# Optimization experiments

Measured on AMD Instinct MI355X. Metric: run time of the kernel, lower is better.

Reference implementation:

```python
import jax, jax.numpy as jnp
import numpy as np

DIM = 1024
HEADS = 16
HEAD_DIM = 64
WINDOW = 64


def setup_inputs() -> dict:
    key = jax.random.key(0)
    ks = jax.random.split(key, 9)
    s = lambda fan_in: 1.0 / np.sqrt(fan_in)
    x = jax.random.normal(ks[0], (2, 2048, DIM), dtype=jnp.float32)
    # KANEXLayer: phi = Linear(dim, hidden=dim) -> SiLU -> Linear(dim, dim); g = Linear(dim, 3*H*D)
    W1 = jax.random.uniform(ks[1], (DIM, DIM), jnp.float32, -s(DIM), s(DIM))
    b1 = jax.random.uniform(ks[2], (DIM,), jnp.float32, -s(DIM), s(DIM))
    W2 = jax.random.uniform(ks[3], (DIM, DIM), jnp.float32, -s(DIM), s(DIM))
    b2 = jax.random.uniform(ks[4], (DIM,), jnp.float32, -s(DIM), s(DIM))
    Wg = jax.random.uniform(ks[5], (3 * HEADS * HEAD_DIM, DIM), jnp.float32, -s(DIM), s(DIM))
    bg = jax.random.uniform(ks[6], (3 * HEADS * HEAD_DIM,), jnp.float32, -s(DIM), s(DIM))
    Wo = jax.random.uniform(ks[7], (DIM, HEADS * HEAD_DIM), jnp.float32, -s(HEADS * HEAD_DIM), s(HEADS * HEAD_DIM))
    bo = jax.random.uniform(ks[8], (DIM,), jnp.float32, -s(HEADS * HEAD_DIM), s(HEADS * HEAD_DIM))
    return {"x": x, "W1": W1, "b1": b1, "W2": W2, "b2": b2,
            "Wg": Wg, "bg": bg, "Wo": Wo, "bo": bo}


def reference(x, W1, b1, W2, b2, Wg, bg, Wo, bo):
    b, n, _ = x.shape
    # KANEXLayer: g(phi(x))
    h = jax.nn.silu(x @ W1.T + b1) @ W2.T + b2          # [b, n, dim]
    qkv = h @ Wg.T + bg                                  # [b, n, 3*H*D]
    q, k, v = jnp.split(qkv, 3, axis=-1)
    reshape = lambda t: t.reshape(b, n, HEADS, HEAD_DIM).transpose(0, 2, 1, 3)  # [b, H, n, D]
    q, k, v = reshape(q), reshape(k), reshape(v)
    dots = jnp.einsum('bhid,bhjd->bhij', q, k) * (HEAD_DIM ** -0.5)  # [b, H, n, n]
    # mask positions j >= i + window (triu with diagonal=window_size)
    i = jnp.arange(n)[:, None]
    j = jnp.arange(n)[None, :]
    mask = j >= i + WINDOW                               # [n, n] bool
    dots = jnp.where(mask, -jnp.inf, dots)
    attn = jax.nn.softmax(dots, axis=-1)
    out = jnp.einsum('bhij,bhjd->bhid', attn, v)         # [b, H, n, D]
    out = out.transpose(0, 2, 1, 3).reshape(b, n, HEADS * HEAD_DIM)
    return out @ Wo.T + bo                               # [b, n, dim]
```

## Files before the change

kernel.cpp:

```cpp
#include <hip/hip_runtime.h>

typedef unsigned short u16;
typedef unsigned int   u32;
typedef __bf16 bf16x8 __attribute__((ext_vector_type(8)));
typedef float  f32x4  __attribute__((ext_vector_type(4)));

__device__ __forceinline__ u16 f2bf(float f) {
    return __builtin_bit_cast(u16, (__bf16)f);
}

__device__ __forceinline__ void gload16(const void* g, void* lds) {
    __builtin_amdgcn_global_load_lds(
        (const __attribute__((address_space(1))) u32*)g,
        (__attribute__((address_space(3))) u32*)lds, 16, 0, 0);
}

__device__ __forceinline__ f32x4 mfma16(bf16x8 a, bf16x8 b, f32x4 c) {
    return __builtin_amdgcn_mfma_f32_16x16x32_bf16(a, b, c, 0, 0, 0);
}

__global__ __launch_bounds__(256) void k_cvt5(const float* __restrict__ x,
                                              const float* __restrict__ W1,
                                              const float* __restrict__ W2,
                                              const float* __restrict__ Wg,
                                              const float* __restrict__ Wo,
                                              u16* __restrict__ xb, u16* __restrict__ w1b,
                                              u16* __restrict__ w2b, u16* __restrict__ wgb,
                                              u16* __restrict__ wob) {
    int i = blockIdx.x * 256 + threadIdx.x;
    const float* src; u16* dst; int off;
    if (i < 1048576)      { src = x;  dst = xb;  off = 0; }
    else if (i < 1310720) { src = W1; dst = w1b; off = 1048576; }
    else if (i < 1572864) { src = W2; dst = w2b; off = 1310720; }
    else if (i < 2359296) { src = Wg; dst = wgb; off = 1572864; }
    else                  { src = Wo; dst = wob; off = 2359296; }
    int j = i - off;
    float4 v = ((const float4*)src)[j];
    ushort4 o;
    o.x = f2bf(v.x); o.y = f2bf(v.y); o.z = f2bf(v.z); o.w = f2bf(v.w);
    ((ushort4*)dst)[j] = o;
}

template<bool SILU, bool OUT_BF16>
__global__ __launch_bounds__(512) void k_gemm(const u16* __restrict__ A,
                                              const u16* __restrict__ B,
                                              const float* __restrict__ bias,
                                              void* __restrict__ Cout,
                                              int M, int N, int K, int qcols) {
    __shared__ __align__(16) u16 As[2][128 * 64];
    __shared__ __align__(16) u16 Bs[2][128 * 64];
    const int tid = threadIdx.x;
    const int w = tid >> 6, l = tid & 63;
    const int wm = w >> 2, wn = w & 3;
    const int lr = l & 15, lg = l >> 4;

    const int nwg = gridDim.x * gridDim.y;
    const int hw = blockIdx.x + gridDim.x * blockIdx.y;
    const int wg = (hw & 7) * (nwg >> 3) + (hw >> 3);
    const int m0 = (wg % gridDim.x) * 128, n0 = (wg / gridDim.x) * 128;

    f32x4 acc[4][2];
#pragma unroll
    for (int i = 0; i < 4; ++i)
#pragma unroll
        for (int j = 0; j < 2; ++j) acc[i][j] = (f32x4){0.f, 0.f, 0.f, 0.f};

    const int srow = l >> 3;
    const int ss = (l & 7) ^ (srow & 7);
    auto STAGE = [&](int buf, int kt) {
#pragma unroll
        for (int i = 0; i < 4; ++i) {
            const int g = w * 4 + i;
            if (g < 16)
                gload16(&A[(size_t)(m0 + g * 8 + srow) * K + kt * 64 + ss * 8],
                        &As[buf][g * 512]);
            else
                gload16(&B[(size_t)(n0 + (g - 16) * 8 + srow) * K + kt * 64 + ss * 8],
                        &Bs[buf][(g - 16) * 512]);
        }
    };

    const int nkt = K >> 6;
    STAGE(0, 0);
    __syncthreads();
    for (int kt = 0; kt < nkt; ++kt) {
        const int cur = kt & 1;
        if (kt + 1 < nkt) STAGE(cur ^ 1, kt + 1);
#pragma unroll
        for (int s = 0; s < 2; ++s) {
            bf16x8 af[4], bq[2];
#pragma unroll
            for (int f = 0; f < 4; ++f) {
                const int r = wm * 64 + f * 16 + lr;
                af[f] = *(const bf16x8*)&As[cur][r * 64 + (((s * 4 + lg) ^ (r & 7)) * 8)];
            }
#pragma unroll
            for (int n = 0; n < 2; ++n) {
                const int r = wn * 32 + n * 16 + lr;
                bq[n] = *(const bf16x8*)&Bs[cur][r * 64 + (((s * 4 + lg) ^ (r & 7)) * 8)];
            }
#pragma unroll
            for (int mf = 0; mf < 4; ++mf)
#pragma unroll
                for (int nf = 0; nf < 2; ++nf)
                    acc[mf][nf] = mfma16(af[mf], bq[nf], acc[mf][nf]);
        }
        if (kt + 1 < nkt) __syncthreads();
    }

#pragma unroll
    for (int nf = 0; nf < 2; ++nf) {
        const int col = n0 + wn * 32 + nf * 16 + lr;
        const float bv = bias[col];
        const float cs = (col < qcols) ? 0.18033688011112042f : 1.0f;
#pragma unroll
        for (int mf = 0; mf < 4; ++mf) {
#pragma unroll
            for (int r = 0; r < 4; ++r) {
                const int row = m0 + wm * 64 + mf * 16 + lg * 4 + r;
                float v = acc[mf][nf][r] + bv;
                if (SILU) v = v / (1.0f + __expf(-v));
                v *= cs;
                if (OUT_BF16) ((u16*)Cout)[(size_t)row * N + col] = f2bf(v);
                else          ((float*)Cout)[(size_t)row * N + col] = v;
            }
        }
    }
}

__global__ __launch_bounds__(256) void k_vt(const u16* __restrict__ qkv,
                                            u16* __restrict__ vt) {
    __shared__ u16 tile[64][66];
    const int bh = blockIdx.y;
    const int b = bh >> 4, h = bh & 15;
    const int n0 = blockIdx.x * 64;
    const int tid = threadIdx.x;
#pragma unroll
    for (int it = 0; it < 16; ++it) {
        int idx = it * 256 + tid;
        int r = idx >> 6, c = idx & 63;
        tile[r][c] = qkv[(size_t)(b * 2048 + n0 + r) * 3072 + 2048 + h * 64 + c];
    }
    __syncthreads();
#pragma unroll
    for (int it = 0; it < 16; ++it) {
        int idx = it * 256 + tid;
        int d = idx >> 6, c = idx & 63;
        vt[(size_t)(bh * 64 + d) * 2048 + n0 + c] = tile[c][d];
    }
}

__device__ __forceinline__ void attn_leg(const u16* __restrict__ Ksb,
                                         const u16* __restrict__ Vsb,
                                         u16* __restrict__ Plw,
                                         int lr, int lg, bf16x8 q0, bf16x8 q1,
                                         f32x4 (&o)[4], float& ls,
                                         int thr, bool domask) {
    f32x4 st[4];
#pragma unroll
    for (int f = 0; f < 4; ++f) st[f] = (f32x4){0.f, 0.f, 0.f, 0.f};
    __builtin_amdgcn_s_setprio(1);
#pragma unroll
    for (int s = 0; s < 2; ++s) {
        const bf16x8 qf = s ? q1 : q0;
#pragma unroll
        for (int f = 0; f < 4; ++f) {
            const int row = f * 16 + lr;
            const int sw = ((s * 4 + lg) ^ (row & 7)) * 8;
            bf16x8 kf = *(const bf16x8*)&Ksb[row * 64 + sw];
            st[f] = mfma16(kf, qf, st[f]);
        }
    }
    __builtin_amdgcn_s_setprio(0);
    const int kbase = lg * 4;
#pragma unroll
    for (int f = 0; f < 4; ++f) {
        float pv[4];
#pragma unroll
        for (int r = 0; r < 4; ++r) {
            float sv = st[f][r];
            if (domask) sv = (f * 16 + kbase + r > thr) ? -1e30f : sv;
            pv[r] = exp2f(sv);
            ls += pv[r];
        }
        ushort4 pw;
        pw.x = f2bf(pv[0]); pw.y = f2bf(pv[1]); pw.z = f2bf(pv[2]); pw.w = f2bf(pv[3]);
        *(ushort4*)&Plw[lr * 80 + f * 16 + kbase] = pw;
    }
    __builtin_amdgcn_s_setprio(1);
#pragma unroll
    for (int s = 0; s < 2; ++s) {
        const bf16x8 pf = *(const bf16x8*)&Plw[lr * 80 + s * 32 + lg * 8];
#pragma unroll
        for (int f = 0; f < 4; ++f) {
            const int row = f * 16 + lr;
            const int sw = ((s * 4 + lg) ^ (row & 7)) * 8;
            bf16x8 vf = *(const bf16x8*)&Vsb[row * 64 + sw];
            o[f] = mfma16(pf, vf, o[f]);
        }
    }
    __builtin_amdgcn_s_setprio(0);
}

__global__ __launch_bounds__(512) void k_attn(const u16* __restrict__ qkv,
                                              const u16* __restrict__ vt,
                                              u16* __restrict__ ao) {
    __shared__ __align__(16) u16 Ks[2][64 * 64];
    __shared__ __align__(16) u16 Vs[2][64 * 64];
    __shared__ __align__(16) u16 Pl[8][16 * 80];
    const int hw = blockIdx.x + 16 * blockIdx.y;
    const int logical = (hw & 7) * 64 + (hw >> 3);
    const int p = logical & 15, bh = logical >> 4;
    const int b = bh >> 4, h = bh & 15;
    const int tid = threadIdx.x, w = tid >> 6, l = tid & 63;
    const int lr = l & 15, lg = l >> 4;
    const int i = (w >> 2) ? (31 - p) : p;
    const int nt = min(i + 2, 32);
    const int ntL = min(33 - p, 32);

    const size_t qb = (size_t)(b * 2048 + i * 64 + (w & 3) * 16 + lr) * 3072 + h * 64;
    const bf16x8 q0 = *(const bf16x8*)&qkv[qb + lg * 8];
    const bf16x8 q1 = *(const bf16x8*)&qkv[qb + 32 + lg * 8];

    f32x4 o[4];
#pragma unroll
    for (int f = 0; f < 4; ++f) o[f] = (f32x4){0.f, 0.f, 0.f, 0.f};
    float ls = 0.f;
    const int ql = i * 64 + (w & 3) * 16 + lr;

    const int srow = tid >> 3;
    const int ss = (tid & 7) ^ (srow & 7);
    auto STAGE = [&](int buf, int t) {
        const int j0 = t * 64;
        gload16(&qkv[(size_t)(b * 2048 + j0 + srow) * 3072 + 1024 + h * 64 + ss * 8],
                &Ks[buf][tid * 8]);
        gload16(&vt[(size_t)(bh * 64 + srow) * 2048 + j0 + ss * 8], &Vs[buf][tid * 8]);
    };

    STAGE(0, 0);
    __syncthreads();
    for (int t = 0; t < ntL; ++t) {
        const int cur = t & 1;
        if (t + 1 < ntL) STAGE(cur ^ 1, t + 1);
        if (t < nt)
            attn_leg(Ks[cur], Vs[cur], Pl[w], lr, lg, q0, q1, o, ls,
                     ql + 63 - t * 64, t == nt - 1);
        __syncthreads();
    }

    ls += __shfl_xor(ls, 16); ls += __shfl_xor(ls, 32);
    float li[4];
#pragma unroll
    for (int r = 0; r < 4; ++r) li[r] = 1.0f / __shfl(ls, lg * 4 + r);
#pragma unroll
    for (int f = 0; f < 4; ++f) {
#pragma unroll
        for (int r = 0; r < 4; ++r) {
            const int row = b * 2048 + i * 64 + (w & 3) * 16 + lg * 4 + r;
            ao[(size_t)row * 1024 + h * 64 + f * 16 + lr] = f2bf(o[f][r] * li[r]);
        }
    }
}

extern "C" void kernel_launch(void* const* d_in, const int* in_sizes, int n_in,
                              void* d_out, int out_size, void* d_ws, size_t ws_size,
                              hipStream_t stream) {
    const float* x  = (const float*)d_in[0];
    const float* W1 = (const float*)d_in[1];
    const float* b1 = (const float*)d_in[2];
    const float* W2 = (const float*)d_in[3];
    const float* b2 = (const float*)d_in[4];
    const float* Wg = (const float*)d_in[5];
    const float* bg = (const float*)d_in[6];
    const float* Wo = (const float*)d_in[7];
    const float* bo = (const float*)d_in[8];
    float* out = (float*)d_out;

    char* ws = (char*)d_ws;
    const size_t MB = 1024 * 1024;
    u16* x_bf   = (u16*)(ws + 0);
    u16* w1_bf  = (u16*)(ws + 8  * MB);
    u16* w2_bf  = (u16*)(ws + 10 * MB);
    u16* wg_bf  = (u16*)(ws + 12 * MB);
    u16* wo_bf  = (u16*)(ws + 18 * MB);
    u16* h1_bf  = (u16*)(ws + 20 * MB);
    u16* h_bf   = (u16*)(ws + 28 * MB);
    u16* qkv_bf = (u16*)(ws + 36 * MB);
    u16* vt_bf  = (u16*)(ws + 60 * MB);
    u16* ao_bf  = (u16*)(ws + 68 * MB);

    k_cvt5<<<10240, 256, 0, stream>>>(x, W1, W2, Wg, Wo,
                                      x_bf, w1_bf, w2_bf, wg_bf, wo_bf);

    k_gemm<true,  true ><<<dim3(32, 8),  512, 0, stream>>>(x_bf,  w1_bf, b1, h1_bf,  4096, 1024, 1024, 0);
    k_gemm<false, true ><<<dim3(32, 8),  512, 0, stream>>>(h1_bf, w2_bf, b2, h_bf,   4096, 1024, 1024, 0);
    k_gemm<false, true ><<<dim3(32, 24), 512, 0, stream>>>(h_bf,  wg_bf, bg, qkv_bf, 4096, 3072, 1024, 1024);

    k_vt  <<<dim3(32, 32), 256, 0, stream>>>(qkv_bf, vt_bf);
    k_attn<<<dim3(16, 32), 512, 0, stream>>>(qkv_bf, vt_bf, ao_bf);

    k_gemm<false, false><<<dim3(32, 8), 512, 0, stream>>>(ao_bf, wo_bf, bo, out, 4096, 1024, 1024, 0);
}
```

Before: 158.2 us.

## Rewrite attention with 32x32 MFMA and register-resident P via permlane swaps

```diff
diff --git a/kernel.cpp b/kernel.cpp
--- a/kernel.cpp
+++ b/kernel.cpp
@@ -4,9 +4,17 @@
 typedef unsigned int   u32;
 typedef __bf16 bf16x8 __attribute__((ext_vector_type(8)));
 typedef float  f32x4  __attribute__((ext_vector_type(4)));
+typedef float  f32x16 __attribute__((ext_vector_type(16)));
+typedef u32    u32x4  __attribute__((ext_vector_type(4)));
 
 __device__ __forceinline__ u16 f2bf(float f) {
     return __builtin_bit_cast(u16, (__bf16)f);
+}
+__device__ __forceinline__ u32 pk2(float lo, float hi) {
+    return (u32)f2bf(lo) | ((u32)f2bf(hi) << 16);
+}
+__device__ __forceinline__ void plswap(u32& a, u32& b) {
+    asm volatile("v_permlane32_swap_b32 %0, %1" : "+v"(a), "+v"(b));
 }
 
 __device__ __forceinline__ void gload16(const void* g, void* lds) {
@@ -17,6 +25,9 @@
 
 __device__ __forceinline__ f32x4 mfma16(bf16x8 a, bf16x8 b, f32x4 c) {
     return __builtin_amdgcn_mfma_f32_16x16x32_bf16(a, b, c, 0, 0, 0);
+}
+__device__ __forceinline__ f32x16 mfma32(bf16x8 a, bf16x8 b, f32x16 c) {
+    return __builtin_amdgcn_mfma_f32_32x32x16_bf16(a, b, c, 0, 0, 0);
 }
 
 __global__ __launch_bounds__(256) void k_cvt5(const float* __restrict__ x,
@@ -150,91 +161,43 @@
     }
 }
 
-__device__ __forceinline__ void attn_leg(const u16* __restrict__ Ksb,
-                                         const u16* __restrict__ Vsb,
-                                         u16* __restrict__ Plw,
-                                         int lr, int lg, bf16x8 q0, bf16x8 q1,
-                                         f32x4 (&o)[4], float& ls,
-                                         int thr, bool domask) {
-    f32x4 st[4];
-#pragma unroll
-    for (int f = 0; f < 4; ++f) st[f] = (f32x4){0.f, 0.f, 0.f, 0.f};
-    __builtin_amdgcn_s_setprio(1);
-#pragma unroll
-    for (int s = 0; s < 2; ++s) {
-        const bf16x8 qf = s ? q1 : q0;
-#pragma unroll
-        for (int f = 0; f < 4; ++f) {
-            const int row = f * 16 + lr;
-            const int sw = ((s * 4 + lg) ^ (row & 7)) * 8;
-            bf16x8 kf = *(const bf16x8*)&Ksb[row * 64 + sw];
-            st[f] = mfma16(kf, qf, st[f]);
-        }
-    }
-    __builtin_amdgcn_s_setprio(0);
-    const int kbase = lg * 4;
-#pragma unroll
-    for (int f = 0; f < 4; ++f) {
-        float pv[4];
-#pragma unroll
-        for (int r = 0; r < 4; ++r) {
-            float sv = st[f][r];
-            if (domask) sv = (f * 16 + kbase + r > thr) ? -1e30f : sv;
-            pv[r] = exp2f(sv);
-            ls += pv[r];
-        }
-        ushort4 pw;
-        pw.x = f2bf(pv[0]); pw.y = f2bf(pv[1]); pw.z = f2bf(pv[2]); pw.w = f2bf(pv[3]);
-        *(ushort4*)&Plw[lr * 80 + f * 16 + kbase] = pw;
-    }
-    __builtin_amdgcn_s_setprio(1);
-#pragma unroll
-    for (int s = 0; s < 2; ++s) {
-        const bf16x8 pf = *(const bf16x8*)&Plw[lr * 80 + s * 32 + lg * 8];
-#pragma unroll
-        for (int f = 0; f < 4; ++f) {
-            const int row = f * 16 + lr;
-            const int sw = ((s * 4 + lg) ^ (row & 7)) * 8;
-            bf16x8 vf = *(const bf16x8*)&Vsb[row * 64 + sw];
-            o[f] = mfma16(pf, vf, o[f]);
-        }
-    }
-    __builtin_amdgcn_s_setprio(0);
-}
-
-__global__ __launch_bounds__(512) void k_attn(const u16* __restrict__ qkv,
+__global__ __launch_bounds__(256) void k_attn(const u16* __restrict__ qkv,
                                               const u16* __restrict__ vt,
                                               u16* __restrict__ ao) {
     __shared__ __align__(16) u16 Ks[2][64 * 64];
     __shared__ __align__(16) u16 Vs[2][64 * 64];
-    __shared__ __align__(16) u16 Pl[8][16 * 80];
     const int hw = blockIdx.x + 16 * blockIdx.y;
     const int logical = (hw & 7) * 64 + (hw >> 3);
     const int p = logical & 15, bh = logical >> 4;
     const int b = bh >> 4, h = bh & 15;
     const int tid = threadIdx.x, w = tid >> 6, l = tid & 63;
-    const int lr = l & 15, lg = l >> 4;
-    const int i = (w >> 2) ? (31 - p) : p;
+    const int l31 = l & 31, hi = l >> 5, l7 = l & 7;
+    const int i = (w >> 1) ? (31 - p) : p;
+    const int qsub = (w & 1) * 32;
     const int nt = min(i + 2, 32);
     const int ntL = min(33 - p, 32);
-
-    const size_t qb = (size_t)(b * 2048 + i * 64 + (w & 3) * 16 + lr) * 3072 + h * 64;
-    const bf16x8 q0 = *(const bf16x8*)&qkv[qb + lg * 8];
-    const bf16x8 q1 = *(const bf16x8*)&qkv[qb + 32 + lg * 8];
-
-    f32x4 o[4];
-#pragma unroll
-    for (int f = 0; f < 4; ++f) o[f] = (f32x4){0.f, 0.f, 0.f, 0.f};
+    const int qg = i * 64 + qsub + l31;
+
+    bf16x8 qf[4];
+    const size_t qb = (size_t)(b * 2048 + qg) * 3072 + h * 64 + hi * 8;
+#pragma unroll
+    for (int s = 0; s < 4; ++s) qf[s] = *(const bf16x8*)&qkv[qb + s * 16];
+
+    f32x16 o0 = {}, o1 = {};
     float ls = 0.f;
-    const int ql = i * 64 + (w & 3) * 16 + lr;
-
-    const int srow = tid >> 3;
-    const int ss = (tid & 7) ^ (srow & 7);
+
     auto STAGE = [&](int buf, int t) {
         const int j0 = t * 64;
-        gload16(&qkv[(size_t)(b * 2048 + j0 + srow) * 3072 + 1024 + h * 64 + ss * 8],
-                &Ks[buf][tid * 8]);
-        gload16(&vt[(size_t)(bh * 64 + srow) * 2048 + j0 + ss * 8], &Vs[buf][tid * 8]);
+#pragma unroll
+        for (int it = 0; it < 2; ++it) {
+            const int cbase = it * 256 + w * 64;
+            const int c = cbase + l;
+            const int row = c >> 3, slot = c & 7;
+            const int sw = slot ^ (row & 7);
+            gload16(&qkv[(size_t)(b * 2048 + j0 + row) * 3072 + 1024 + h * 64 + sw * 8],
+                    &Ks[buf][cbase * 8]);
+            gload16(&vt[(size_t)(bh * 64 + row) * 2048 + j0 + sw * 8], &Vs[buf][cbase * 8]);
+        }
     };
 
     STAGE(0, 0);
@@ -242,22 +205,79 @@
     for (int t = 0; t < ntL; ++t) {
         const int cur = t & 1;
         if (t + 1 < ntL) STAGE(cur ^ 1, t + 1);
-        if (t < nt)
-            attn_leg(Ks[cur], Vs[cur], Pl[w], lr, lg, q0, q1, o, ls,
-                     ql + 63 - t * 64, t == nt - 1);
+        if (t < nt) {
+            const u16* Kc = Ks[cur];
+            const u16* Vc = Vs[cur];
+            f32x16 st0 = {}, st1 = {};
+            __builtin_amdgcn_s_setprio(1);
+#pragma unroll
+            for (int s = 0; s < 4; ++s) {
+                const int off = ((2 * s + hi) ^ l7) * 8;
+                bf16x8 k0 = *(const bf16x8*)&Kc[l31 * 64 + off];
+                bf16x8 k1 = *(const bf16x8*)&Kc[(32 + l31) * 64 + off];
+                st0 = mfma32(k0, qf[s], st0);
+                st1 = mfma32(k1, qf[s], st1);
+            }
+            __builtin_amdgcn_s_setprio(0);
+            const bool dm = (t == nt - 1);
+            const int thr = qg + 63 - t * 64;
+            u32 pka[2][8];
+#pragma unroll
+            for (int mf = 0; mf < 2; ++mf) {
+#pragma unroll
+                for (int pp = 0; pp < 8; ++pp) {
+                    const int r0 = 2 * pp;
+                    float e0 = mf ? st1[r0] : st0[r0];
+                    float e1 = mf ? st1[r0 + 1] : st0[r0 + 1];
+                    const int kv0 = 32 * mf + (r0 & 3) + 8 * (r0 >> 2) + 4 * hi;
+                    if (dm) {
+                        e0 = (kv0 > thr) ? -1e30f : e0;
+                        e1 = (kv0 + 1 > thr) ? -1e30f : e1;
+                    }
+                    e0 = exp2f(e0); e1 = exp2f(e1);
+                    ls += e0 + e1;
+                    pka[mf][pp] = pk2(e0, e1);
+                }
+            }
+#pragma unroll
+            for (int mf = 0; mf < 2; ++mf) {
+                plswap(pka[mf][0], pka[mf][2]);
+                plswap(pka[mf][1], pka[mf][3]);
+                plswap(pka[mf][4], pka[mf][6]);
+                plswap(pka[mf][5], pka[mf][7]);
+            }
+            __builtin_amdgcn_s_setprio(1);
+#pragma unroll
+            for (int s = 0; s < 4; ++s) {
+                const int mf = s >> 1, o4 = (s & 1) * 4;
+                u32x4 pu = {pka[mf][o4], pka[mf][o4 + 1], pka[mf][o4 + 2], pka[mf][o4 + 3]};
+                const bf16x8 pa = __builtin_bit_cast(bf16x8, pu);
+                const int off = ((2 * s + hi) ^ l7) * 8;
+                bf16x8 v0 = *(const bf16x8*)&Vc[l31 * 64 + off];
+                bf16x8 v1 = *(const bf16x8*)&Vc[(32 + l31) * 64 + off];
+                o0 = mfma32(v0, pa, o0);
+                o1 = mfma32(v1, pa, o1);
+            }
+            __builtin_amdgcn_s_setprio(0);
+        }
         __syncthreads();
     }
 
-    ls += __shfl_xor(ls, 16); ls += __shfl_xor(ls, 32);
-    float li[4];
-#pragma unroll
-    for (int r = 0; r < 4; ++r) li[r] = 1.0f / __shfl(ls, lg * 4 + r);
-#pragma unroll
-    for (int f = 0; f < 4; ++f) {
-#pragma unroll
-        for (int r = 0; r < 4; ++r) {
-            const int row = b * 2048 + i * 64 + (w & 3) * 16 + lg * 4 + r;
-            ao[(size_t)row * 1024 + h * 64 + f * 16 + lr] = f2bf(o[f][r] * li[r]);
+    ls += __shfl_xor(ls, 32);
+    const float li = 1.0f / ls;
+    const size_t orow = (size_t)(b * 2048 + qg) * 1024 + h * 64;
+#pragma unroll
+    for (int db = 0; db < 2; ++db) {
+#pragma unroll
+        for (int g = 0; g < 4; ++g) {
+            float v0 = (db ? o1[4 * g + 0] : o0[4 * g + 0]) * li;
+            float v1 = (db ? o1[4 * g + 1] : o0[4 * g + 1]) * li;
+            float v2 = (db ? o1[4 * g + 2] : o0[4 * g + 2]) * li;
+            float v3 = (db ? o1[4 * g + 3] : o0[4 * g + 3]) * li;
+            ushort4 pw;
+            pw.x = f2bf(v0); pw.y = f2bf(v1); pw.z = f2bf(v2); pw.w = f2bf(v3);
+            const int d0 = db * 32 + g * 8 + hi * 4;
+            *(ushort4*)&ao[orow + d0] = pw;
         }
     }
 }
@@ -297,7 +317,7 @@
     k_gemm<false, true ><<<dim3(32, 24), 512, 0, stream>>>(h_bf,  wg_bf, bg, qkv_bf, 4096, 3072, 1024, 1024);
 
     k_vt  <<<dim3(32, 32), 256, 0, stream>>>(qkv_bf, vt_bf);
-    k_attn<<<dim3(16, 32), 512, 0, stream>>>(qkv_bf, vt_bf, ao_bf);
+    k_attn<<<dim3(16, 32), 256, 0, stream>>>(qkv_bf, vt_bf, ao_bf);
 
     k_gemm<false, false><<<dim3(32, 8), 512, 0, stream>>>(ao_bf, wo_bf, bo, out, 4096, 1024, 1024, 0);
 }
```

Result: slower. 181.6 us (+14.8%).
